# Performance work log

Hardware: AMD Instinct MI355X
Metric: run time of the kernel (lower is better)

Reference implementation:

```python
import jax, jax.numpy as jnp
import numpy as np

B, S, D = 4, 2048, 1024
H = 4096          # d_model * hidden_mult
E = 8             # n_experts
TOP_K = 2
AUX_COEF = 0.01


def setup_inputs() -> dict:
    key = jax.random.key(0)
    ks = jax.random.split(key, 5)
    x = jax.random.normal(ks[0], (B, S, D), dtype=jnp.float32)
    router_w = jax.random.normal(ks[1], (D, E), dtype=jnp.float32) * 0.02
    temp = jnp.ones((1,), dtype=jnp.float32)
    Wg = jax.random.normal(ks[2], (E, D, H), dtype=jnp.float32) * 0.02
    Wu = jax.random.normal(ks[3], (E, D, H), dtype=jnp.float32) * 0.02
    Wd = jax.random.normal(ks[4], (E, H, D), dtype=jnp.float32) * 0.02
    return {"x": x, "router_w": router_w, "temp": temp, "Wg": Wg, "Wu": Wu, "Wd": Wd}


def reference(x, router_w, temp, Wg, Wu, Wd):
    # --- Top2Router (eval mode: no jitter noise, no dropout) ---
    t = jnp.clip(temp, 0.1, 5.0)                         # scalar temp param, clamped
    logits = jnp.einsum('bsd,de->bse', x, router_w) / t   # [B,S,E]
    probs = jax.nn.softmax(logits, axis=-1)
    w, idx = jax.lax.top_k(probs, TOP_K)                  # [B,S,K] weights / expert ids

    # --- Expert dispatch / compute / combine ---
    # dropless=True -> no capacity dropping. Tokens not routed to expert e get
    # combine weight 0, so a masked-weight dense accumulate matches the
    # gather->MLP->scatter math of the original exactly.
    out = jnp.zeros_like(x)
    for e in range(E):  # fixed small expert count; structurally distinct weights
        we = jnp.sum(w * (idx == e), axis=-1)             # [B,S] combine weight for expert e
        gate = jnp.einsum('bsd,dh->bsh', x, Wg[e])
        up = jnp.einsum('bsd,dh->bsh', x, Wu[e])
        hidden = jax.nn.silu(up) * gate                   # swiglu: silu(up_proj) * gate_proj
        ye = jnp.einsum('bsh,hd->bsd', hidden, Wd[e])
        out = out + we[..., None] * ye

    # --- Aux losses ---
    importance = probs.mean(axis=(0, 1))                  # [E]
    assigned = jnp.sum(jax.nn.one_hot(idx, E, dtype=probs.dtype), axis=(0, 1, 2))  # [E]
    load = assigned / (B * S + 1e-6)
    aux_load_loss = (importance * load).sum() * E * AUX_COEF
    router_entropy = -(probs * jnp.log(jnp.clip(probs, 1e-8))).sum(-1).mean() * 0.01
    overflow_pct = jnp.zeros((), dtype=x.dtype)           # dropless -> never overflows
    return out, aux_load_loss, router_entropy, overflow_pct
```

## Files before the change

### kernel.cpp

```cpp
#include <hip/hip_runtime.h>
#include <stdint.h>

#define T_TOK 8192
#define D_DIM 1024
#define H_DIM 4096
#define NGU   8192
#define NEXP  8
#define MAX_YT 136

typedef float  f32x4  __attribute__((ext_vector_type(4)));
typedef __bf16 bf16x8 __attribute__((ext_vector_type(8)));
typedef __bf16 bf16x4 __attribute__((ext_vector_type(4)));

__device__ __forceinline__ void gl_lds16(const void* g, void* l) {
  __builtin_amdgcn_global_load_lds(
      (__attribute__((address_space(1))) void*)g,
      (__attribute__((address_space(3))) void*)l, 16u, 0, 0u);
}

__global__ __launch_bounds__(256) void router_kernel(
    const float* __restrict__ x, const float* __restrict__ rw,
    const float* __restrict__ temp, __bf16* __restrict__ xb,
    int* __restrict__ rowtok, float* __restrict__ rowwt,
    int* __restrict__ cnt, float* __restrict__ imp_part,
    float* __restrict__ ent_part)
{
  const int wid  = threadIdx.x >> 6;
  const int lane = threadIdx.x & 63;
  const int t    = blockIdx.x * 4 + wid;

  float acc[8];
#pragma unroll
  for (int e = 0; e < 8; e++) acc[e] = 0.f;
  const float* xr = x + (size_t)t * D_DIM;
#pragma unroll
  for (int it = 0; it < 4; it++) {
    int d = (it * 64 + lane) * 4;
    float4 v = *(const float4*)(xr + d);
    bf16x4 o;
    o[0] = (__bf16)v.x; o[1] = (__bf16)v.y;
    o[2] = (__bf16)v.z; o[3] = (__bf16)v.w;
    *(bf16x4*)(xb + (size_t)t * D_DIM + d) = o;
    float vv[4] = {v.x, v.y, v.z, v.w};
#pragma unroll
    for (int j = 0; j < 4; j++) {
      float xv = vv[j];
      const float4 r0 = *(const float4*)(rw + (d + j) * 8);
      const float4 r1 = *(const float4*)(rw + (d + j) * 8 + 4);
      acc[0] += xv * r0.x; acc[1] += xv * r0.y;
      acc[2] += xv * r0.z; acc[3] += xv * r0.w;
      acc[4] += xv * r1.x; acc[5] += xv * r1.y;
      acc[6] += xv * r1.z; acc[7] += xv * r1.w;
    }
  }
#pragma unroll
  for (int e = 0; e < 8; e++) {
    float v = acc[e];
#pragma unroll
    for (int off = 32; off > 0; off >>= 1) v += __shfl_xor(v, off, 64);
    acc[e] = v;
  }
  float tclamp = fminf(fmaxf(temp[0], 0.1f), 5.0f);
  float invt = 1.0f / tclamp;
  float mx = -1e30f;
#pragma unroll
  for (int e = 0; e < 8; e++) { acc[e] *= invt; mx = fmaxf(mx, acc[e]); }
  float p[8]; float s = 0.f;
#pragma unroll
  for (int e = 0; e < 8; e++) { p[e] = __expf(acc[e] - mx); s += p[e]; }
  float invs = 1.0f / s;
  float ent = 0.f;
#pragma unroll
  for (int e = 0; e < 8; e++) {
    p[e] *= invs;
    ent -= p[e] * __logf(fmaxf(p[e], 1e-8f));
  }
  int i1 = 0; float w1 = p[0];
#pragma unroll
  for (int e = 1; e < 8; e++) if (p[e] > w1) { w1 = p[e]; i1 = e; }
  int i2 = (i1 == 0) ? 1 : 0; float w2 = p[i2];
#pragma unroll
  for (int e = 0; e < 8; e++) if (e != i1 && p[e] > w2) { w2 = p[e]; i2 = e; }

  __shared__ float s_imp[4][8];
  __shared__ float s_ent[4];
  if (lane == 0) {
    int pos1 = atomicAdd(&cnt[i1], 1);
    rowtok[i1 * T_TOK + pos1] = t * 2;
    rowwt [i1 * T_TOK + pos1] = w1;
    int pos2 = atomicAdd(&cnt[i2], 1);
    rowtok[i2 * T_TOK + pos2] = t * 2 + 1;
    rowwt [i2 * T_TOK + pos2] = w2;
#pragma unroll
    for (int e = 0; e < 8; e++) s_imp[wid][e] = p[e];
    s_ent[wid] = ent;
  }
  __syncthreads();
  if (threadIdx.x < 8) {
    int e = threadIdx.x;
    imp_part[blockIdx.x * 8 + e] =
        s_imp[0][e] + s_imp[1][e] + s_imp[2][e] + s_imp[3][e];
  } else if (threadIdx.x == 8) {
    ent_part[blockIdx.x] = s_ent[0] + s_ent[1] + s_ent[2] + s_ent[3];
  }
}

__global__ __launch_bounds__(256) void aux_final_kernel(
    const float* __restrict__ imp_part, const float* __restrict__ ent_part,
    const int* __restrict__ cnt, int* __restrict__ tileoff,
    float* __restrict__ out_aux)
{
  __shared__ float simp[256];
  __shared__ float sent[256];
  int tid = threadIdx.x;
  int e = tid & 7, g = tid >> 3;
  float ia = 0.f;
  for (int b = g; b < 2048; b += 32) ia += imp_part[b * 8 + e];
  simp[tid] = ia;
  float ea = 0.f;
  for (int b = tid; b < 2048; b += 256) ea += ent_part[b];
  sent[tid] = ea;
  __syncthreads();
  if (tid == 0) {
    float imp[8] = {0,0,0,0,0,0,0,0};
    float ent = 0.f;
    for (int i = 0; i < 256; i++) { imp[i & 7] += simp[i]; ent += sent[i]; }
    float aux = 0.f;
    for (int ee = 0; ee < 8; ee++) {
      float importance = imp[ee] / 8192.0f;
      float load = (float)cnt[ee] / (8192.0f + 1e-6f);
      aux += importance * load;
    }
    out_aux[0] = aux * 8.0f * 0.01f;
    out_aux[1] = (ent / 8192.0f) * 0.01f;
    out_aux[2] = 0.f;
    int off = 0;
    for (int ee = 0; ee < 8; ee++) { tileoff[ee] = off; off += (cnt[ee] + 127) >> 7; }
    tileoff[8] = off;
  }
}

__global__ __launch_bounds__(256) void transpose_all_kernel(
    const float* __restrict__ Wg, const float* __restrict__ Wu,
    const float* __restrict__ Wd,
    __bf16* __restrict__ BguT, __bf16* __restrict__ BdT)
{
  __shared__ float tile[64 * 129];
  int z = blockIdx.z;
  const float* src; __bf16* dst;
  int C, Kd, r0, c0, up = 0;
  bool gu = z < 16;
  if (gu) {
    int e = z >> 1; up = z & 1;
    src = (up ? Wu : Wg) + (size_t)e * D_DIM * H_DIM;
    dst = BguT + (size_t)e * NGU * D_DIM;
    C = H_DIM; Kd = D_DIM;
    c0 = (blockIdx.x & 31) << 7;  r0 = (blockIdx.x >> 5) << 6;
  } else {
    int e = z - 16;
    src = Wd + (size_t)e * H_DIM * D_DIM;
    dst = BdT + (size_t)e * D_DIM * H_DIM;
    C = D_DIM; Kd = H_DIM;
    c0 = (blockIdx.x & 7) << 7;   r0 = (blockIdx.x >> 3) << 6;
  }
  int t = threadIdx.x;
  int cq = t & 31, rb = t >> 5;
#pragma unroll
  for (int i = 0; i < 8; i++) {
    int r = rb + 8 * i;
    float4 v = *(const float4*)(src + (size_t)(r0 + r) * C + c0 + cq * 4);
    *(float4*)&tile[r * 129 + cq * 4] = v;
  }
  __syncthreads();
#pragma unroll
  for (int i = 0; i < 4; i++) {
    int c = t + (i << 8);
    int hl = c >> 3;
    int rc = c & 7;
    int dstrow;
    if (gu) { int h = c0 + hl; dstrow = ((h >> 4) << 5) + (h & 15) + (up << 4); }
    else    { dstrow = c0 + hl; }
    bf16x8 o;
#pragma unroll
    for (int j = 0; j < 8; j++)
      o[j] = (__bf16)tile[(rc * 8 + j) * 129 + hl];
    *(bf16x8*)(dst + (size_t)dstrow * Kd + r0 + rc * 8) = o;
  }
}

__global__ __launch_bounds__(256, 2) void gemm1_kernel(
    const __bf16* __restrict__ xb, const __bf16* __restrict__ BguT,
    const int* __restrict__ rowtok, const float* __restrict__ rowwt,
    const int* __restrict__ cnt, const int* __restrict__ tileoff,
    __bf16* __restrict__ hid)
{
  __shared__ __bf16 As[128 * 64];
  __shared__ __bf16 Bs[128 * 64];
  __shared__ int   s_tok[128];
  __shared__ float s_wt[128];

  int y = blockIdx.y;
  if (y >= tileoff[8]) return;
  int e = 0;
  while (y >= tileoff[e + 1]) e++;
  int m0 = (y - tileoff[e]) << 7;
  int cntE = cnt[e];
  int tid = threadIdx.x;
  if (tid < 128) {
    int m = m0 + tid;
    bool v = m < cntE;
    s_tok[tid] = v ? rowtok[e * T_TOK + m] : 0;
    s_wt [tid] = v ? rowwt [e * T_TOK + m] : 0.f;
  }
  __syncthreads();

  const int n0 = blockIdx.x << 7;
  const __bf16* Bp = BguT + (size_t)e * NGU * D_DIM;
  const int lane = tid & 63;
  const int wid = tid >> 6;
  const int wm = wid >> 1, wn = wid & 1;
  const int l15 = lane & 15, l4 = lane >> 4;

  f32x4 zero = {0.f, 0.f, 0.f, 0.f};
  f32x4 acc[4][4];
#pragma unroll
  for (int a = 0; a < 4; a++)
#pragma unroll
    for (int b = 0; b < 4; b++) acc[a][b] = zero;

  int q[4], ar[4], akc[4];
#pragma unroll
  for (int c = 0; c < 4; c++) {
    q[c]   = tid + (c << 8);
    ar[c]  = q[c] >> 3;
    akc[c] = ((q[c] & 7) ^ (ar[c] & 7)) << 3;
  }

  for (int kt = 0; kt < 16; kt++) {
    int k0 = kt << 6;
#pragma unroll
    for (int c = 0; c < 4; c++) {
      const __bf16* ga = xb + (size_t)(s_tok[ar[c]] >> 1) * D_DIM + (k0 + akc[c]);
      gl_lds16(ga, &As[q[c] << 3]);
    }
#pragma unroll
    for (int c = 0; c < 4; c++) {
      const __bf16* gb = Bp + (size_t)(n0 + ar[c]) * D_DIM + (k0 + akc[c]);
      gl_lds16(gb, &Bs[q[c] << 3]);
    }
    __syncthreads();
#pragma unroll
    for (int ks = 0; ks < 2; ks++) {
      bf16x8 af[4], bfv[4];
#pragma unroll
      for (int mi = 0; mi < 4; mi++) {
        int row = wm * 64 + mi * 16 + l15;
        int kidx = (ks * 4 + l4) ^ (row & 7);
        af[mi] = *(const bf16x8*)&As[(row * 8 + kidx) * 8];
      }
#pragma unroll
      for (int ni = 0; ni < 4; ni++) {
        int row = wn * 64 + ni * 16 + l15;
        int kidx = (ks * 4 + l4) ^ (row & 7);
        bfv[ni] = *(const bf16x8*)&Bs[(row * 8 + kidx) * 8];
      }
#pragma unroll
      for (int mi = 0; mi < 4; mi++)
#pragma unroll
        for (int ni = 0; ni < 4; ni++)
          acc[mi][ni] = __builtin_amdgcn_mfma_f32_16x16x32_bf16(
              af[mi], bfv[ni], acc[mi][ni], 0, 0, 0);
    }
    __syncthreads();
  }

#pragma unroll
  for (int mi = 0; mi < 4; mi++) {
#pragma unroll
    for (int p2 = 0; p2 < 2; p2++) {
      f32x4 gt = acc[mi][2 * p2];
      f32x4 up = acc[mi][2 * p2 + 1];
      int nb = n0 + wn * 64 + p2 * 32;
      int h = ((nb >> 5) << 4) + l15;
#pragma unroll
      for (int r = 0; r < 4; r++) {
        int rl = wm * 64 + mi * 16 + l4 * 4 + r;
        if (m0 + rl < cntE) {
          float u = up[r];
          float hv = (u / (1.f + __expf(-u))) * gt[r] * s_wt[rl];
          hid[(size_t)s_tok[rl] * H_DIM + h] = (__bf16)hv;
        }
      }
    }
  }
}

__global__ __launch_bounds__(256, 2) void gemm2_kernel(
    const __bf16* __restrict__ hid, const __bf16* __restrict__ BdT,
    const int* __restrict__ rowtok, const int* __restrict__ cnt,
    const int* __restrict__ tileoff, float* __restrict__ ytmp)
{
  __shared__ __bf16 As[128 * 64];
  __shared__ __bf16 Bs[128 * 64];
  __shared__ int s_tok[128];

  int y = blockIdx.y;
  if (y >= tileoff[8]) return;
  int e = 0;
  while (y >= tileoff[e + 1]) e++;
  int m0 = (y - tileoff[e]) << 7;
  int cntE = cnt[e];
  int tid = threadIdx.x;
  if (tid < 128) {
    int m = m0 + tid;
    s_tok[tid] = (m < cntE) ? rowtok[e * T_TOK + m] : 0;
  }
  __syncthreads();

  const int n0 = blockIdx.x << 7;
  const __bf16* Bp = BdT + (size_t)e * D_DIM * H_DIM;
  const int lane = tid & 63;
  const int wid = tid >> 6;
  const int wm = wid >> 1, wn = wid & 1;
  const int l15 = lane & 15, l4 = lane >> 4;

  f32x4 zero = {0.f, 0.f, 0.f, 0.f};
  f32x4 acc[4][4];
#pragma unroll
  for (int a = 0; a < 4; a++)
#pragma unroll
    for (int b = 0; b < 4; b++) acc[a][b] = zero;

  int q[4], ar[4], akc[4];
#pragma unroll
  for (int c = 0; c < 4; c++) {
    q[c]   = tid + (c << 8);
    ar[c]  = q[c] >> 3;
    akc[c] = ((q[c] & 7) ^ (ar[c] & 7)) << 3;
  }

  for (int kt = 0; kt < 64; kt++) {
    int k0 = kt << 6;
#pragma unroll
    for (int c = 0; c < 4; c++) {
      const __bf16* ga = hid + (size_t)s_tok[ar[c]] * H_DIM + (k0 + akc[c]);
      gl_lds16(ga, &As[q[c] << 3]);
    }
#pragma unroll
    for (int c = 0; c < 4; c++) {
      const __bf16* gb = Bp + (size_t)(n0 + ar[c]) * H_DIM + (k0 + akc[c]);
      gl_lds16(gb, &Bs[q[c] << 3]);
    }
    __syncthreads();
#pragma unroll
    for (int ks = 0; ks < 2; ks++) {
      bf16x8 af[4], bfv[4];
#pragma unroll
      for (int mi = 0; mi < 4; mi++) {
        int row = wm * 64 + mi * 16 + l15;
        int kidx = (ks * 4 + l4) ^ (row & 7);
        af[mi] = *(const bf16x8*)&As[(row * 8 + kidx) * 8];
      }
#pragma unroll
      for (int ni = 0; ni < 4; ni++) {
        int row = wn * 64 + ni * 16 + l15;
        int kidx = (ks * 4 + l4) ^ (row & 7);
        bfv[ni] = *(const bf16x8*)&Bs[(row * 8 + kidx) * 8];
      }
#pragma unroll
      for (int mi = 0; mi < 4; mi++)
#pragma unroll
        for (int ni = 0; ni < 4; ni++)
          acc[mi][ni] = __builtin_amdgcn_mfma_f32_16x16x32_bf16(
              af[mi], bfv[ni], acc[mi][ni], 0, 0, 0);
    }
    __syncthreads();
  }

#pragma unroll
  for (int mi = 0; mi < 4; mi++)
#pragma unroll
    for (int ni = 0; ni < 4; ni++) {
      int coln = n0 + wn * 64 + ni * 16 + l15;
#pragma unroll
      for (int r = 0; r < 4; r++) {
        int rl = wm * 64 + mi * 16 + l4 * 4 + r;
        if (m0 + rl < cntE)
          ytmp[(size_t)s_tok[rl] * D_DIM + coln] = acc[mi][ni][r];
      }
    }
}

__global__ __launch_bounds__(256) void combine_kernel(
    const float* __restrict__ ytmp, float* __restrict__ out)
{
  size_t i = ((size_t)blockIdx.x * 256 + threadIdx.x) * 4;
  size_t t = i >> 10;
  size_t col = i & 1023;
  const float4 a = *(const float4*)(ytmp + ((t * 2) << 10) + col);
  const float4 b = *(const float4*)(ytmp + ((t * 2 + 1) << 10) + col);
  float4 o = {a.x + b.x, a.y + b.y, a.z + b.z, a.w + b.w};
  *(float4*)(out + i) = o;
}

extern "C" void kernel_launch(void* const* d_in, const int* in_sizes, int n_in,
                              void* d_out, int out_size, void* d_ws, size_t ws_size,
                              hipStream_t stream)
{
  const float* x    = (const float*)d_in[0];
  const float* rw   = (const float*)d_in[1];
  const float* temp = (const float*)d_in[2];
  const float* Wg   = (const float*)d_in[3];
  const float* Wu   = (const float*)d_in[4];
  const float* Wd   = (const float*)d_in[5];
  float* out = (float*)d_out;

  char* ws = (char*)d_ws;
  size_t off = 0;
  auto alloc = [&](size_t bytes) -> void* {
    void* p = ws + off;
    off = (off + bytes + 255) & ~(size_t)255;
    return p;
  };
  __bf16* xb     = (__bf16*)alloc((size_t)T_TOK * D_DIM * 2);
  __bf16* BguT   = (__bf16*)alloc((size_t)NEXP * NGU * D_DIM * 2);
  __bf16* BdT    = (__bf16*)alloc((size_t)NEXP * D_DIM * H_DIM * 2);
  __bf16* hid    = (__bf16*)alloc((size_t)T_TOK * 2 * H_DIM * 2);
  int*    rowtok = (int*)  alloc((size_t)NEXP * T_TOK * 4);
  float*  rowwt  = (float*)alloc((size_t)NEXP * T_TOK * 4);
  int*    cnt    = (int*)  alloc(64);
  int*    tileoff= (int*)  alloc(64);
  float*  imp_part = (float*)alloc(2048 * 8 * 4);
  float*  ent_part = (float*)alloc(2048 * 4);
  float* ytmp = (float*)BguT;
  (void)ws_size; (void)n_in; (void)in_sizes;

  hipMemsetAsync(cnt, 0, 64, stream);

  router_kernel<<<2048, 256, 0, stream>>>(x, rw, temp, xb, rowtok, rowwt, cnt,
                                          imp_part, ent_part);
  aux_final_kernel<<<1, 256, 0, stream>>>(imp_part, ent_part, cnt, tileoff,
                                          out + (size_t)T_TOK * D_DIM);
  transpose_all_kernel<<<dim3(512, 1, 24), 256, 0, stream>>>(Wg, Wu, Wd,
                                                             BguT, BdT);
  gemm1_kernel<<<dim3(64, MAX_YT), 256, 0, stream>>>(xb, BguT, rowtok, rowwt,
                                                     cnt, tileoff, hid);
  gemm2_kernel<<<dim3(8, MAX_YT), 256, 0, stream>>>(hid, BdT, rowtok, cnt,
                                                    tileoff, ytmp);
  combine_kernel<<<8192, 256, 0, stream>>>(ytmp, out);
}
```

Baseline: 1.132 ms.

## Use 256x256 double-buffered pipelined MFMA tiles and split-K for down projection

```diff
diff --git a/kernel.cpp b/kernel.cpp
--- a/kernel.cpp
+++ b/kernel.cpp
@@ -6,7 +6,7 @@
 #define H_DIM 4096
 #define NGU   8192
 #define NEXP  8
-#define MAX_YT 136
+#define MAX_YT 72
 
 typedef float  f32x4  __attribute__((ext_vector_type(4)));
 typedef __bf16 bf16x8 __attribute__((ext_vector_type(8)));
@@ -17,6 +17,14 @@
       (__attribute__((address_space(1))) void*)g,
       (__attribute__((address_space(3))) void*)l, 16u, 0, 0u);
 }
+
+#define SFENCE() __builtin_amdgcn_sched_barrier(0)
+#define BARRIER() do { SFENCE(); __builtin_amdgcn_s_barrier(); SFENCE(); } while (0)
+#define VM0 asm volatile("s_waitcnt vmcnt(0)" ::: "memory")
+#define VM4 asm volatile("s_waitcnt vmcnt(4)" ::: "memory")
+#define VM6 asm volatile("s_waitcnt vmcnt(6)" ::: "memory")
+#define VM8 asm volatile("s_waitcnt vmcnt(8)" ::: "memory")
+#define VM_NONE ((void)0)
 
 __global__ __launch_bounds__(256) void router_kernel(
     const float* __restrict__ x, const float* __restrict__ rw,
@@ -135,7 +143,7 @@
     out_aux[1] = (ent / 8192.0f) * 0.01f;
     out_aux[2] = 0.f;
     int off = 0;
-    for (int ee = 0; ee < 8; ee++) { tileoff[ee] = off; off += (cnt[ee] + 127) >> 7; }
+    for (int ee = 0; ee < 8; ee++) { tileoff[ee] = off; off += (cnt[ee] + 255) >> 8; }
     tileoff[8] = off;
   }
 }
@@ -188,25 +196,81 @@
   }
 }
 
-__global__ __launch_bounds__(256, 2) void gemm1_kernel(
+
+#define STAGE_A0(tt, NTT) do { if ((tt) < (NTT)) {                             \
+    int b_ = (tt) & 1; int k_ = (tt) << 6;                                     \
+    gl_lds16(aptr[0] + k_, &As[b_][aoff]);                                     \
+    gl_lds16(aptr[2] + k_, &As[b_][aoff + 2 * 4096]); } } while (0)
+#define STAGE_A1(tt, NTT) do { if ((tt) < (NTT)) {                             \
+    int b_ = (tt) & 1; int k_ = (tt) << 6;                                     \
+    gl_lds16(aptr[1] + k_, &As[b_][aoff + 1 * 4096]);                          \
+    gl_lds16(aptr[3] + k_, &As[b_][aoff + 3 * 4096]); } } while (0)
+#define STAGE_B0(tt, NTT) do { if ((tt) < (NTT)) {                             \
+    int b_ = (tt) & 1; int k_ = (tt) << 6;                                     \
+    gl_lds16(bptr[0] + k_, &Bs[b_][boff0]);                                    \
+    gl_lds16(bptr[2] + k_, &Bs[b_][boff2]); } } while (0)
+#define STAGE_B1(tt, NTT) do { if ((tt) < (NTT)) {                             \
+    int b_ = (tt) & 1; int k_ = (tt) << 6;                                     \
+    gl_lds16(bptr[1] + k_, &Bs[b_][boff1]);                                    \
+    gl_lds16(bptr[3] + k_, &Bs[b_][boff3]); } } while (0)
+
+#define PHASE(QM, QN, STAGE_STMT, WAIT_STMT) do {                              \
+  bf16x8 af_[4][2], bf_[2][2];                                                 \
+  _Pragma("unroll")                                                            \
+  for (int mi_ = 0; mi_ < 4; mi_++) {                                          \
+    int r_ = wm * 128 + (QM) * 64 + mi_ * 16 + l15;                            \
+    _Pragma("unroll")                                                          \
+    for (int kk_ = 0; kk_ < 2; kk_++) {                                        \
+      int kx_ = (kk_ * 4 + l4) ^ (r_ & 7);                                     \
+      af_[mi_][kk_] = *(const bf16x8*)&Ac[(r_ * 8 + kx_) * 8];                 \
+    }                                                                          \
+  }                                                                            \
+  _Pragma("unroll")                                                            \
+  for (int ni_ = 0; ni_ < 2; ni_++) {                                          \
+    int r_ = wn * 64 + (QN) * 32 + ni_ * 16 + l15;                             \
+    _Pragma("unroll")                                                          \
+    for (int kk_ = 0; kk_ < 2; kk_++) {                                        \
+      int kx_ = (kk_ * 4 + l4) ^ (r_ & 7);                                     \
+      bf_[ni_][kk_] = *(const bf16x8*)&Bc[(r_ * 8 + kx_) * 8];                 \
+    }                                                                          \
+  }                                                                            \
+  STAGE_STMT;                                                                  \
+  BARRIER();                                                                   \
+  __builtin_amdgcn_s_setprio(1);                                               \
+  _Pragma("unroll")                                                            \
+  for (int kk_ = 0; kk_ < 2; kk_++)                                            \
+    _Pragma("unroll")                                                          \
+    for (int mi_ = 0; mi_ < 4; mi_++)                                          \
+      _Pragma("unroll")                                                        \
+      for (int ni_ = 0; ni_ < 2; ni_++)                                        \
+        acc[(QM) * 4 + mi_][(QN) * 2 + ni_] =                                  \
+            __builtin_amdgcn_mfma_f32_16x16x32_bf16(                           \
+                af_[mi_][kk_], bf_[ni_][kk_],                                  \
+                acc[(QM) * 4 + mi_][(QN) * 2 + ni_], 0, 0, 0);                 \
+  __builtin_amdgcn_s_setprio(0);                                               \
+  WAIT_STMT;                                                                   \
+  BARRIER();                                                                   \
+} while (0)
+
+__global__ __launch_bounds__(512, 2) void gemm1_kernel(
     const __bf16* __restrict__ xb, const __bf16* __restrict__ BguT,
     const int* __restrict__ rowtok, const float* __restrict__ rowwt,
     const int* __restrict__ cnt, const int* __restrict__ tileoff,
     __bf16* __restrict__ hid)
 {
-  __shared__ __bf16 As[128 * 64];
-  __shared__ __bf16 Bs[128 * 64];
-  __shared__ int   s_tok[128];
-  __shared__ float s_wt[128];
+  __shared__ __bf16 As[2][256 * 64];
+  __shared__ __bf16 Bs[2][256 * 64];
+  __shared__ int   s_tok[256];
+  __shared__ float s_wt[256];
 
   int y = blockIdx.y;
   if (y >= tileoff[8]) return;
   int e = 0;
   while (y >= tileoff[e + 1]) e++;
-  int m0 = (y - tileoff[e]) << 7;
+  int m0 = (y - tileoff[e]) << 8;
   int cntE = cnt[e];
   int tid = threadIdx.x;
-  if (tid < 128) {
+  if (tid < 256) {
     int m = m0 + tid;
     bool v = m < cntE;
     s_tok[tid] = v ? rowtok[e * T_TOK + m] : 0;
@@ -214,68 +278,65 @@
   }
   __syncthreads();
 
-  const int n0 = blockIdx.x << 7;
+  const int n0 = blockIdx.x << 8;
   const __bf16* Bp = BguT + (size_t)e * NGU * D_DIM;
   const int lane = tid & 63;
-  const int wid = tid >> 6;
-  const int wm = wid >> 1, wn = wid & 1;
+  const int wid  = tid >> 6;
+  const int wm = wid >> 2, wn = wid & 3;
   const int l15 = lane & 15, l4 = lane >> 4;
 
-  f32x4 zero = {0.f, 0.f, 0.f, 0.f};
-  f32x4 acc[4][4];
-#pragma unroll
-  for (int a = 0; a < 4; a++)
-#pragma unroll
-    for (int b = 0; b < 4; b++) acc[a][b] = zero;
-
-  int q[4], ar[4], akc[4];
-#pragma unroll
-  for (int c = 0; c < 4; c++) {
-    q[c]   = tid + (c << 8);
-    ar[c]  = q[c] >> 3;
-    akc[c] = ((q[c] & 7) ^ (ar[c] & 7)) << 3;
-  }
-
-  for (int kt = 0; kt < 16; kt++) {
-    int k0 = kt << 6;
-#pragma unroll
-    for (int c = 0; c < 4; c++) {
-      const __bf16* ga = xb + (size_t)(s_tok[ar[c]] >> 1) * D_DIM + (k0 + akc[c]);
-      gl_lds16(ga, &As[q[c] << 3]);
-    }
-#pragma unroll
-    for (int c = 0; c < 4; c++) {
-      const __bf16* gb = Bp + (size_t)(n0 + ar[c]) * D_DIM + (k0 + akc[c]);
-      gl_lds16(gb, &Bs[q[c] << 3]);
-    }
-    __syncthreads();
-#pragma unroll
-    for (int ks = 0; ks < 2; ks++) {
-      bf16x8 af[4], bfv[4];
-#pragma unroll
-      for (int mi = 0; mi < 4; mi++) {
-        int row = wm * 64 + mi * 16 + l15;
-        int kidx = (ks * 4 + l4) ^ (row & 7);
-        af[mi] = *(const bf16x8*)&As[(row * 8 + kidx) * 8];
-      }
-#pragma unroll
-      for (int ni = 0; ni < 4; ni++) {
-        int row = wn * 64 + ni * 16 + l15;
-        int kidx = (ks * 4 + l4) ^ (row & 7);
-        bfv[ni] = *(const bf16x8*)&Bs[(row * 8 + kidx) * 8];
-      }
-#pragma unroll
-      for (int mi = 0; mi < 4; mi++)
-#pragma unroll
-        for (int ni = 0; ni < 4; ni++)
-          acc[mi][ni] = __builtin_amdgcn_mfma_f32_16x16x32_bf16(
-              af[mi], bfv[ni], acc[mi][ni], 0, 0, 0);
-    }
-    __syncthreads();
-  }
-
-#pragma unroll
-  for (int mi = 0; mi < 4; mi++) {
+  const int rr = tid >> 3, ch = tid & 7;
+  const int swz = (ch ^ (rr & 7)) << 3;
+  const int rB = rr + ((rr >> 5) << 5);
+  const int aoff = rr * 64 + ch * 8;
+
+  const __bf16* aptr[4];
+#pragma unroll
+  for (int Q = 0; Q < 4; Q++)
+    aptr[Q] = xb + (size_t)(s_tok[Q * 64 + rr] >> 1) * D_DIM + swz;
+  const __bf16* bptr[4];
+  const int bb0 = 0, bb1 = 32, bb2 = 128, bb3 = 160;
+  bptr[0] = Bp + (size_t)(n0 + bb0 + rB) * D_DIM + swz;
+  bptr[1] = Bp + (size_t)(n0 + bb1 + rB) * D_DIM + swz;
+  bptr[2] = Bp + (size_t)(n0 + bb2 + rB) * D_DIM + swz;
+  bptr[3] = Bp + (size_t)(n0 + bb3 + rB) * D_DIM + swz;
+  const int boff0 = (bb0 + rB) * 64 + ch * 8;
+  const int boff1 = (bb1 + rB) * 64 + ch * 8;
+  const int boff2 = (bb2 + rB) * 64 + ch * 8;
+  const int boff3 = (bb3 + rB) * 64 + ch * 8;
+
+  f32x4 acc[8][4];
+#pragma unroll
+  for (int a = 0; a < 8; a++)
+#pragma unroll
+    for (int b = 0; b < 4; b++) acc[a][b] = (f32x4){0.f, 0.f, 0.f, 0.f};
+
+  STAGE_A0(0, 16); STAGE_B0(0, 16); STAGE_A1(0, 16); STAGE_B1(0, 16);
+  STAGE_A0(1, 16); STAGE_B0(1, 16);
+  VM8;
+  BARRIER();
+
+  for (int t = 0; t < 15; t++) {
+    const __bf16* Ac = &As[t & 1][0];
+    const __bf16* Bc = &Bs[t & 1][0];
+    PHASE(0, 0, STAGE_A1(t + 1, 16), VM6);
+    PHASE(0, 1, STAGE_B1(t + 1, 16), VM_NONE);
+    PHASE(1, 0, STAGE_A0(t + 2, 16), VM_NONE);
+    PHASE(1, 1, STAGE_B0(t + 2, 16), VM8);
+  }
+  VM4;
+  BARRIER();
+  {
+    const __bf16* Ac = &As[1][0];
+    const __bf16* Bc = &Bs[1][0];
+    PHASE(0, 0, VM_NONE, VM0);
+    PHASE(0, 1, VM_NONE, VM_NONE);
+    PHASE(1, 0, VM_NONE, VM_NONE);
+    PHASE(1, 1, VM_NONE, VM_NONE);
+  }
+
+#pragma unroll
+  for (int mi = 0; mi < 8; mi++) {
 #pragma unroll
     for (int p2 = 0; p2 < 2; p2++) {
       f32x4 gt = acc[mi][2 * p2];
@@ -284,7 +345,7 @@
       int h = ((nb >> 5) << 4) + l15;
 #pragma unroll
       for (int r = 0; r < 4; r++) {
-        int rl = wm * 64 + mi * 16 + l4 * 4 + r;
+        int rl = wm * 128 + mi * 16 + l4 * 4 + r;
         if (m0 + rl < cntE) {
           float u = up[r];
           float hv = (u / (1.f + __expf(-u))) * gt[r] * s_wt[rl];
@@ -295,98 +356,97 @@
   }
 }
 
-__global__ __launch_bounds__(256, 2) void gemm2_kernel(
+__global__ __launch_bounds__(512, 2) void gemm2_kernel(
     const __bf16* __restrict__ hid, const __bf16* __restrict__ BdT,
     const int* __restrict__ rowtok, const int* __restrict__ cnt,
     const int* __restrict__ tileoff, float* __restrict__ ytmp)
 {
-  __shared__ __bf16 As[128 * 64];
-  __shared__ __bf16 Bs[128 * 64];
-  __shared__ int s_tok[128];
+  __shared__ __bf16 As[2][256 * 64];
+  __shared__ __bf16 Bs[2][256 * 64];
+  __shared__ int s_tok[256];
 
   int y = blockIdx.y;
   if (y >= tileoff[8]) return;
   int e = 0;
   while (y >= tileoff[e + 1]) e++;
-  int m0 = (y - tileoff[e]) << 7;
+  int m0 = (y - tileoff[e]) << 8;
   int cntE = cnt[e];
   int tid = threadIdx.x;
-  if (tid < 128) {
+  if (tid < 256) {
     int m = m0 + tid;
     s_tok[tid] = (m < cntE) ? rowtok[e * T_TOK + m] : 0;
   }
   __syncthreads();
 
-  const int n0 = blockIdx.x << 7;
+  const int n0 = blockIdx.x << 8;
+  const int kz = blockIdx.z << 11;
   const __bf16* Bp = BdT + (size_t)e * D_DIM * H_DIM;
   const int lane = tid & 63;
-  const int wid = tid >> 6;
-  const int wm = wid >> 1, wn = wid & 1;
+  const int wid  = tid >> 6;
+  const int wm = wid >> 2, wn = wid & 3;
   const int l15 = lane & 15, l4 = lane >> 4;
 
-  f32x4 zero = {0.f, 0.f, 0.f, 0.f};
-  f32x4 acc[4][4];
-#pragma unroll
-  for (int a = 0; a < 4; a++)
-#pragma unroll
-    for (int b = 0; b < 4; b++) acc[a][b] = zero;
-
-  int q[4], ar[4], akc[4];
-#pragma unroll
-  for (int c = 0; c < 4; c++) {
-    q[c]   = tid + (c << 8);
-    ar[c]  = q[c] >> 3;
-    akc[c] = ((q[c] & 7) ^ (ar[c] & 7)) << 3;
-  }
-
-  for (int kt = 0; kt < 64; kt++) {
-    int k0 = kt << 6;
-#pragma unroll
-    for (int c = 0; c < 4; c++) {
-      const __bf16* ga = hid + (size_t)s_tok[ar[c]] * H_DIM + (k0 + akc[c]);
-      gl_lds16(ga, &As[q[c] << 3]);
-    }
-#pragma unroll
-    for (int c = 0; c < 4; c++) {
-      const __bf16* gb = Bp + (size_t)(n0 + ar[c]) * H_DIM + (k0 + akc[c]);
-      gl_lds16(gb, &Bs[q[c] << 3]);
-    }
-    __syncthreads();
-#pragma unroll
-    for (int ks = 0; ks < 2; ks++) {
-      bf16x8 af[4], bfv[4];
-#pragma unroll
-      for (int mi = 0; mi < 4; mi++) {
-        int row = wm * 64 + mi * 16 + l15;
-        int kidx = (ks * 4 + l4) ^ (row & 7);
-        af[mi] = *(const bf16x8*)&As[(row * 8 + kidx) * 8];
-      }
-#pragma unroll
-      for (int ni = 0; ni < 4; ni++) {
-        int row = wn * 64 + ni * 16 + l15;
-        int kidx = (ks * 4 + l4) ^ (row & 7);
-        bfv[ni] = *(const bf16x8*)&Bs[(row * 8 + kidx) * 8];
-      }
-#pragma unroll
-      for (int mi = 0; mi < 4; mi++)
-#pragma unroll
-        for (int ni = 0; ni < 4; ni++)
-          acc[mi][ni] = __builtin_amdgcn_mfma_f32_16x16x32_bf16(
-              af[mi], bfv[ni], acc[mi][ni], 0, 0, 0);
-    }
-    __syncthreads();
-  }
-
-#pragma unroll
-  for (int mi = 0; mi < 4; mi++)
-#pragma unroll
-    for (int ni = 0; ni < 4; ni++) {
-      int coln = n0 + wn * 64 + ni * 16 + l15;
+  const int rr = tid >> 3, ch = tid & 7;
+  const int swz = (ch ^ (rr & 7)) << 3;
+  const int rB = rr + ((rr >> 5) << 5);
+  const int aoff = rr * 64 + ch * 8;
+
+  const __bf16* aptr[4];
+#pragma unroll
+  for (int Q = 0; Q < 4; Q++)
+    aptr[Q] = hid + (size_t)s_tok[Q * 64 + rr] * H_DIM + kz + swz;
+  const __bf16* bptr[4];
+  const int bb0 = 0, bb1 = 32, bb2 = 128, bb3 = 160;
+  bptr[0] = Bp + (size_t)(n0 + bb0 + rB) * H_DIM + kz + swz;
+  bptr[1] = Bp + (size_t)(n0 + bb1 + rB) * H_DIM + kz + swz;
+  bptr[2] = Bp + (size_t)(n0 + bb2 + rB) * H_DIM + kz + swz;
+  bptr[3] = Bp + (size_t)(n0 + bb3 + rB) * H_DIM + kz + swz;
+  const int boff0 = (bb0 + rB) * 64 + ch * 8;
+  const int boff1 = (bb1 + rB) * 64 + ch * 8;
+  const int boff2 = (bb2 + rB) * 64 + ch * 8;
+  const int boff3 = (bb3 + rB) * 64 + ch * 8;
+
+  f32x4 acc[8][4];
+#pragma unroll
+  for (int a = 0; a < 8; a++)
+#pragma unroll
+    for (int b = 0; b < 4; b++) acc[a][b] = (f32x4){0.f, 0.f, 0.f, 0.f};
+
+  STAGE_A0(0, 32); STAGE_B0(0, 32); STAGE_A1(0, 32); STAGE_B1(0, 32);
+  STAGE_A0(1, 32); STAGE_B0(1, 32);
+  VM8;
+  BARRIER();
+
+  for (int t = 0; t < 31; t++) {
+    const __bf16* Ac = &As[t & 1][0];
+    const __bf16* Bc = &Bs[t & 1][0];
+    PHASE(0, 0, STAGE_A1(t + 1, 32), VM6);
+    PHASE(0, 1, STAGE_B1(t + 1, 32), VM_NONE);
+    PHASE(1, 0, STAGE_A0(t + 2, 32), VM_NONE);
+    PHASE(1, 1, STAGE_B0(t + 2, 32), VM8);
+  }
+  VM4;
+  BARRIER();
+  {
+    const __bf16* Ac = &As[1][0];
+    const __bf16* Bc = &Bs[1][0];
+    PHASE(0, 0, VM_NONE, VM0);
+    PHASE(0, 1, VM_NONE, VM_NONE);
+    PHASE(1, 0, VM_NONE, VM_NONE);
+    PHASE(1, 1, VM_NONE, VM_NONE);
+  }
+
+  float* yz = ytmp + (size_t)blockIdx.z * (2 * T_TOK) * D_DIM;
+#pragma unroll
+  for (int mi = 0; mi < 8; mi++)
+#pragma unroll
+    for (int nj = 0; nj < 4; nj++) {
+      int coln = n0 + wn * 64 + nj * 16 + l15;
 #pragma unroll
       for (int r = 0; r < 4; r++) {
-        int rl = wm * 64 + mi * 16 + l4 * 4 + r;
+        int rl = wm * 128 + mi * 16 + l4 * 4 + r;
         if (m0 + rl < cntE)
-          ytmp[(size_t)s_tok[rl] * D_DIM + coln] = acc[mi][ni][r];
+          yz[(size_t)s_tok[rl] * D_DIM + coln] = acc[mi][nj][r];
       }
     }
 }
@@ -397,9 +457,13 @@
   size_t i = ((size_t)blockIdx.x * 256 + threadIdx.x) * 4;
   size_t t = i >> 10;
   size_t col = i & 1023;
+  const size_t HZ = (size_t)(2 * T_TOK) * D_DIM;
   const float4 a = *(const float4*)(ytmp + ((t * 2) << 10) + col);
   const float4 b = *(const float4*)(ytmp + ((t * 2 + 1) << 10) + col);
-  float4 o = {a.x + b.x, a.y + b.y, a.z + b.z, a.w + b.w};
+  const float4 c = *(const float4*)(ytmp + HZ + ((t * 2) << 10) + col);
+  const float4 d = *(const float4*)(ytmp + HZ + ((t * 2 + 1) << 10) + col);
+  float4 o = {a.x + b.x + c.x + d.x, a.y + b.y + c.y + d.y,
+              a.z + b.z + c.z + d.z, a.w + b.w + c.w + d.w};
   *(float4*)(out + i) = o;
 }
 
@@ -443,9 +507,9 @@
                                           out + (size_t)T_TOK * D_DIM);
   transpose_all_kernel<<<dim3(512, 1, 24), 256, 0, stream>>>(Wg, Wu, Wd,
                                                              BguT, BdT);
-  gemm1_kernel<<<dim3(64, MAX_YT), 256, 0, stream>>>(xb, BguT, rowtok, rowwt,
+  gemm1_kernel<<<dim3(32, MAX_YT), 512, 0, stream>>>(xb, BguT, rowtok, rowwt,
                                                      cnt, tileoff, hid);
-  gemm2_kernel<<<dim3(8, MAX_YT), 256, 0, stream>>>(hid, BdT, rowtok, cnt,
-                                                    tileoff, ytmp);
+  gemm2_kernel<<<dim3(4, MAX_YT, 2), 512, 0, stream>>>(hid, BdT, rowtok, cnt,
+                                                       tileoff, ytmp);
   combine_kernel<<<8192, 256, 0, stream>>>(ytmp, out);
 }
```

Result: slower. 1.350 ms (+19.3%).

## Fuse combine into gemm2 via atomics and XCD-aware block remapping

Applied to the files above, without the earlier changes.

```diff
diff --git a/kernel.cpp b/kernel.cpp
--- a/kernel.cpp
+++ b/kernel.cpp
@@ -199,7 +199,12 @@
   __shared__ int   s_tok[128];
   __shared__ float s_wt[128];
 
-  int y = blockIdx.y;
+  const int nblk8 = (64 * MAX_YT) >> 3;
+  int hwlin = blockIdx.y * 64 + blockIdx.x;
+  int lin = (hwlin & 7) * nblk8 + (hwlin >> 3);
+  int y  = lin >> 6;
+  int bx = lin & 63;
+
   if (y >= tileoff[8]) return;
   int e = 0;
   while (y >= tileoff[e + 1]) e++;
@@ -214,7 +219,7 @@
   }
   __syncthreads();
 
-  const int n0 = blockIdx.x << 7;
+  const int n0 = bx << 7;
   const __bf16* Bp = BguT + (size_t)e * NGU * D_DIM;
   const int lane = tid & 63;
   const int wid = tid >> 6;
@@ -298,13 +303,18 @@
 __global__ __launch_bounds__(256, 2) void gemm2_kernel(
     const __bf16* __restrict__ hid, const __bf16* __restrict__ BdT,
     const int* __restrict__ rowtok, const int* __restrict__ cnt,
-    const int* __restrict__ tileoff, float* __restrict__ ytmp)
+    const int* __restrict__ tileoff, float* __restrict__ out)
 {
   __shared__ __bf16 As[128 * 64];
   __shared__ __bf16 Bs[128 * 64];
   __shared__ int s_tok[128];
 
-  int y = blockIdx.y;
+  const int nblk8 = (8 * MAX_YT) >> 3;
+  int hwlin = blockIdx.y * 8 + blockIdx.x;
+  int lin = (hwlin & 7) * nblk8 + (hwlin >> 3);
+  int y  = lin >> 3;
+  int bx = lin & 7;
+
   if (y >= tileoff[8]) return;
   int e = 0;
   while (y >= tileoff[e + 1]) e++;
@@ -317,7 +327,7 @@
   }
   __syncthreads();
 
-  const int n0 = blockIdx.x << 7;
+  const int n0 = bx << 7;
   const __bf16* Bp = BdT + (size_t)e * D_DIM * H_DIM;
   const int lane = tid & 63;
   const int wid = tid >> 6;
@@ -386,21 +396,10 @@
       for (int r = 0; r < 4; r++) {
         int rl = wm * 64 + mi * 16 + l4 * 4 + r;
         if (m0 + rl < cntE)
-          ytmp[(size_t)s_tok[rl] * D_DIM + coln] = acc[mi][ni][r];
-      }
-    }
-}
-
-__global__ __launch_bounds__(256) void combine_kernel(
-    const float* __restrict__ ytmp, float* __restrict__ out)
-{
-  size_t i = ((size_t)blockIdx.x * 256 + threadIdx.x) * 4;
-  size_t t = i >> 10;
-  size_t col = i & 1023;
-  const float4 a = *(const float4*)(ytmp + ((t * 2) << 10) + col);
-  const float4 b = *(const float4*)(ytmp + ((t * 2 + 1) << 10) + col);
-  float4 o = {a.x + b.x, a.y + b.y, a.z + b.z, a.w + b.w};
-  *(float4*)(out + i) = o;
+          atomicAdd(&out[(size_t)(s_tok[rl] >> 1) * D_DIM + coln],
+                    acc[mi][ni][r]);
+      }
+    }
 }
 
 extern "C" void kernel_launch(void* const* d_in, const int* in_sizes, int n_in,
@@ -432,10 +431,10 @@
   int*    tileoff= (int*)  alloc(64);
   float*  imp_part = (float*)alloc(2048 * 8 * 4);
   float*  ent_part = (float*)alloc(2048 * 4);
-  float* ytmp = (float*)BguT;
   (void)ws_size; (void)n_in; (void)in_sizes;
 
   hipMemsetAsync(cnt, 0, 64, stream);
+  hipMemsetAsync(out, 0, (size_t)T_TOK * D_DIM * sizeof(float), stream);
 
   router_kernel<<<2048, 256, 0, stream>>>(x, rw, temp, xb, rowtok, rowwt, cnt,
                                           imp_part, ent_part);
@@ -446,6 +445,5 @@
   gemm1_kernel<<<dim3(64, MAX_YT), 256, 0, stream>>>(xb, BguT, rowtok, rowwt,
                                                      cnt, tileoff, hid);
   gemm2_kernel<<<dim3(8, MAX_YT), 256, 0, stream>>>(hid, BdT, rowtok, cnt,
-                                                    tileoff, ytmp);
-  combine_kernel<<<8192, 256, 0, stream>>>(ytmp, out);
-}
+                                                    tileoff, out);
+}
```

Result: slower. 1.168 ms (+3.2%).
